# Kernel tuning notes

Measured on AMD Instinct MI355X. Metric: run time of the kernel, lower is better.

The kernel has to match this reference:

```python
import jax, jax.numpy as jnp
import numpy as np
import math

B, S, D, H, FF = 2, 2048, 1024, 16, 4096
DH = D // H


def _layernorm(x, g, b, eps=1e-5):
    mu = jnp.mean(x, axis=-1, keepdims=True)
    var = jnp.mean((x - mu) ** 2, axis=-1, keepdims=True)
    return (x - mu) * jax.lax.rsqrt(var + eps) * g + b


def setup_inputs() -> dict:
    key = jax.random.key(0)
    ks = jax.random.split(key, 16)
    sc = 0.02
    inp = {
        "x": jax.random.normal(ks[0], (B, S, D), dtype=jnp.float32),
        "Wq": jax.random.normal(ks[1], (D, D), dtype=jnp.float32) * sc,
        "bq": jnp.zeros((D,), jnp.float32),
        "Wk": jax.random.normal(ks[2], (D, D), dtype=jnp.float32) * sc,
        "bk": jnp.zeros((D,), jnp.float32),
        "Wv": jax.random.normal(ks[3], (D, D), dtype=jnp.float32) * sc,
        "bv": jnp.zeros((D,), jnp.float32),
        "Wo": jax.random.normal(ks[4], (D, D), dtype=jnp.float32) * sc,
        "bo": jnp.zeros((D,), jnp.float32),
        "Er": jax.random.uniform(ks[5], (S, DH), dtype=jnp.float32),  # torch.rand init
        "W1": jax.random.normal(ks[6], (D, FF), dtype=jnp.float32) * sc,
        "b1": jnp.zeros((FF,), jnp.float32),
        "W2": jax.random.normal(ks[7], (FF, D), dtype=jnp.float32) * sc,
        "b2": jnp.zeros((D,), jnp.float32),
        "g1": jnp.ones((D,), jnp.float32),
        "be1": jnp.zeros((D,), jnp.float32),
        "g2": jnp.ones((D,), jnp.float32),
        "be2": jnp.zeros((D,), jnp.float32),
    }
    return inp


def _skew(qer, m):
    # qer: (B,H,S,S); m: (S,S) flipped upper-triangular mask
    qer = qer * m
    qer = jnp.pad(qer, ((0, 0), (0, 0), (0, 0), (1, 0)))  # (B,H,S,S+1)
    qer = qer.reshape(B, H, S + 1, S)
    return qer[:, :, 1:, :]  # (B,H,S,S)


def reference(x, Wq, bq, Wk, bk, Wv, bv, Wo, bo, Er, W1, b1, W2, b2, g1, be1, g2, be2):
    x1 = _layernorm(x, g1, be1)
    q = ((x1 @ Wq + bq) / math.sqrt(DH)).reshape(B, S, H, DH)
    k = (x1 @ Wk + bk).reshape(B, S, H, DH)
    v = (x1 @ Wv + bv).reshape(B, S, H, DH)
    att = jnp.einsum("bshd,bthd->bhst", q, k)  # (B,H,S,S)
    qer = jnp.einsum("bshd,td->bhst", q, Er)   # (B,H,S,S) since S == max_seq_len
    m = jnp.flip(jnp.triu(jnp.ones((S, S), dtype=x.dtype)), axis=0)
    att = att + _skew(qer, m)
    att = jax.nn.softmax(att, axis=-1)
    out = jnp.einsum("bhst,bthd->bshd", att, v).reshape(B, S, D)
    out = out @ Wo + bo
    x2 = x1 + out
    x3 = _layernorm(x2, g2, be2)
    y = x3 + jax.nn.relu(x3 @ W1 + b1) @ W2 + b2
    return y
```

## Files before the change

kernel.cpp:

```cpp
#include <hip/hip_runtime.h>
#include <stdint.h>

typedef unsigned short u16;
typedef __attribute__((ext_vector_type(8))) short short8;
typedef __attribute__((ext_vector_type(8))) __bf16 bf16x8;
typedef __attribute__((ext_vector_type(4))) float floatx4;

#define AS1 __attribute__((address_space(1)))
#define AS3 __attribute__((address_space(3)))

#define QSCALE 0.18033688f

__device__ __forceinline__ u16 f2bf(float f) {
    union { float f; unsigned u; } v; v.f = f;
    return (u16)((v.u + 0x8000u) >> 16);
}

__device__ __forceinline__ void gl_lds16(const void* g, void* lds) {
    __builtin_amdgcn_global_load_lds((const AS1 unsigned int*)(uintptr_t)g,
                                     (AS3 unsigned int*)(uintptr_t)lds, 16, 0, 0);
}

__device__ __forceinline__ floatx4 mfma16(short8 a, short8 b, floatx4 c) {
    return __builtin_amdgcn_mfma_f32_16x16x32_bf16((bf16x8)a, (bf16x8)b, c, 0, 0, 0);
}

__global__ void transpose4_1024(const float* __restrict__ s0, const float* __restrict__ s1,
                                const float* __restrict__ s2, const float* __restrict__ s3,
                                u16* __restrict__ d) {
    __shared__ float tile[32][33];
    const float* srcs[4] = {s0, s1, s2, s3};
    const float* src = srcs[blockIdx.z];
    u16* dst = d + (size_t)blockIdx.z * 1024 * 1024;
    int c0 = blockIdx.x * 32, r0 = blockIdx.y * 32;
    int tx = threadIdx.x, ty = threadIdx.y;
#pragma unroll
    for (int i = 0; i < 4; i++)
        tile[ty + i * 8][tx] = src[(size_t)(r0 + ty + i * 8) * 1024 + c0 + tx];
    __syncthreads();
#pragma unroll
    for (int i = 0; i < 4; i++)
        dst[(size_t)(c0 + ty + i * 8) * 1024 + r0 + tx] = f2bf(tile[tx][ty + i * 8]);
}

__global__ void transpose_f32_to_bf16(const float* __restrict__ src, u16* __restrict__ dst,
                                      int R, int C) {
    __shared__ float tile[32][33];
    int c0 = blockIdx.x * 32, r0 = blockIdx.y * 32;
    int tx = threadIdx.x, ty = threadIdx.y;
#pragma unroll
    for (int i = 0; i < 4; i++)
        tile[ty + i * 8][tx] = src[(size_t)(r0 + ty + i * 8) * C + c0 + tx];
    __syncthreads();
#pragma unroll
    for (int i = 0; i < 4; i++)
        dst[(size_t)(c0 + ty + i * 8) * R + r0 + tx] = f2bf(tile[tx][ty + i * 8]);
}

__global__ void convert_to_bf16(const float* __restrict__ s, u16* __restrict__ d, int n) {
    int i = blockIdx.x * 256 + threadIdx.x;
    if (i < n) d[i] = f2bf(s[i]);
}

__global__ __launch_bounds__(256) void ln_kernel(const float* __restrict__ x,
                                                 const float* __restrict__ g,
                                                 const float* __restrict__ bt,
                                                 float* __restrict__ yf,
                                                 u16* __restrict__ yb) {
    const int row = blockIdx.x, tid = threadIdx.x;
    const float4 xv = ((const float4*)(x + (size_t)row * 1024))[tid];
    float s = xv.x + xv.y + xv.z + xv.w;
    float sq = xv.x * xv.x + xv.y * xv.y + xv.z * xv.z + xv.w * xv.w;
#pragma unroll
    for (int m = 1; m < 64; m <<= 1) { s += __shfl_xor(s, m); sq += __shfl_xor(sq, m); }
    __shared__ float red[8];
    int w = tid >> 6;
    if ((tid & 63) == 0) { red[w] = s; red[4 + w] = sq; }
    __syncthreads();
    s = red[0] + red[1] + red[2] + red[3];
    sq = red[4] + red[5] + red[6] + red[7];
    float mean = s * (1.f / 1024.f);
    float var = sq * (1.f / 1024.f) - mean * mean;
    float rstd = rsqrtf(var + 1e-5f);
    float4 gv = ((const float4*)g)[tid];
    float4 bv = ((const float4*)bt)[tid];
    float4 y;
    y.x = (xv.x - mean) * rstd * gv.x + bv.x;
    y.y = (xv.y - mean) * rstd * gv.y + bv.y;
    y.z = (xv.z - mean) * rstd * gv.z + bv.z;
    y.w = (xv.w - mean) * rstd * gv.w + bv.w;
    ((float4*)(yf + (size_t)row * 1024))[tid] = y;
    ushort4 u;
    u.x = f2bf(y.x); u.y = f2bf(y.y); u.z = f2bf(y.z); u.w = f2bf(y.w);
    ((ushort4*)(yb + (size_t)row * 1024))[tid] = u;
}

template <int EPI>
__global__ __launch_bounds__(256) void gemm_bt(const u16* __restrict__ A,
                                               const u16* __restrict__ Bt,
                                               const float* __restrict__ bias,
                                               u16* __restrict__ outb,
                                               int M, int N, int K) {
    __shared__ __align__(16) u16 As[128 * 32];
    __shared__ __align__(16) u16 Bs[128 * 32];
    const int tid = threadIdx.x;
    const int w = tid >> 6, l = tid & 63, ln = l & 15, quad = l >> 4;
    const int m0 = blockIdx.y * 128, n0 = blockIdx.x * 128;
    const int wm = (w >> 1) * 64, wn = (w & 1) * 64;
    floatx4 acc[4][4] = {};

    for (int k0 = 0; k0 < K; k0 += 32) {
        __syncthreads();
#pragma unroll
        for (int r = 0; r < 2; r++) {
            int c = tid + r * 256;
            int row = c >> 2, ko = (c & 3) * 8;
            gl_lds16(&A[(size_t)(m0 + row) * K + k0 + ko], &As[(w * 64 + r * 256) * 8]);
            gl_lds16(&Bt[(size_t)(n0 + row) * K + k0 + ko], &Bs[(w * 64 + r * 256) * 8]);
        }
        __syncthreads();
        short8 av[4], bv[4];
#pragma unroll
        for (int mt = 0; mt < 4; mt++)
            av[mt] = *(const short8*)&As[(wm + mt * 16 + ln) * 32 + quad * 8];
#pragma unroll
        for (int nt = 0; nt < 4; nt++)
            bv[nt] = *(const short8*)&Bs[(wn + nt * 16 + ln) * 32 + quad * 8];
#pragma unroll
        for (int mt = 0; mt < 4; mt++)
#pragma unroll
            for (int nt = 0; nt < 4; nt++)
                acc[mt][nt] = mfma16(av[mt], bv[nt], acc[mt][nt]);
    }

#pragma unroll
    for (int nt = 0; nt < 4; nt++) {
        int n = n0 + wn + nt * 16 + ln;
        float bval = bias[n];
#pragma unroll
        for (int mt = 0; mt < 4; mt++) {
#pragma unroll
            for (int r = 0; r < 4; r++) {
                int m = m0 + wm + mt * 16 + quad * 4 + r;
                float v = acc[mt][nt][r] + bval;
                outb[(size_t)m * N + n] = f2bf(fmaxf(v, 0.f));
            }
        }
    }
}

__global__ __launch_bounds__(256) void gemm_qkv(const u16* __restrict__ A,
                                                const u16* __restrict__ Bt,
                                                const float* __restrict__ bq,
                                                const float* __restrict__ bk,
                                                const float* __restrict__ bv,
                                                u16* __restrict__ qb,
                                                u16* __restrict__ kb,
                                                u16* __restrict__ vtb) {
    constexpr int K = 1024;
    __shared__ __align__(16) u16 As[128 * 32];
    __shared__ __align__(16) u16 Bs[128 * 32];
    const int tid = threadIdx.x;
    const int w = tid >> 6, l = tid & 63, ln = l & 15, quad = l >> 4;
    const int m0 = blockIdx.y * 128, n0 = blockIdx.x * 128;
    const int wm = (w >> 1) * 64, wn = (w & 1) * 64;
    floatx4 acc[4][4] = {};

    for (int k0 = 0; k0 < K; k0 += 32) {
        __syncthreads();
#pragma unroll
        for (int r = 0; r < 2; r++) {
            int c = tid + r * 256;
            int row = c >> 2, ko = (c & 3) * 8;
            gl_lds16(&A[(size_t)(m0 + row) * K + k0 + ko], &As[(w * 64 + r * 256) * 8]);
            gl_lds16(&Bt[(size_t)(n0 + row) * K + k0 + ko], &Bs[(w * 64 + r * 256) * 8]);
        }
        __syncthreads();
        short8 av[4], bv4[4];
#pragma unroll
        for (int mt = 0; mt < 4; mt++)
            av[mt] = *(const short8*)&As[(wm + mt * 16 + ln) * 32 + quad * 8];
#pragma unroll
        for (int nt = 0; nt < 4; nt++)
            bv4[nt] = *(const short8*)&Bs[(wn + nt * 16 + ln) * 32 + quad * 8];
#pragma unroll
        for (int mt = 0; mt < 4; mt++)
#pragma unroll
            for (int nt = 0; nt < 4; nt++)
                acc[mt][nt] = mfma16(av[mt], bv4[nt], acc[mt][nt]);
    }

    const int seg = (n0 + wn) >> 10;
#pragma unroll
    for (int nt = 0; nt < 4; nt++) {
        int nl = (n0 + wn + nt * 16 + ln) & 1023;
        float bval = seg == 0 ? bq[nl] : (seg == 1 ? bk[nl] : bv[nl]);
#pragma unroll
        for (int mt = 0; mt < 4; mt++) {
#pragma unroll
            for (int r = 0; r < 4; r++) {
                int m = m0 + wm + mt * 16 + quad * 4 + r;
                float v = acc[mt][nt][r] + bval;
                if (seg == 0) {
                    qb[(size_t)m * 1024 + nl] = f2bf(v * QSCALE);
                } else if (seg == 1) {
                    kb[(size_t)m * 1024 + nl] = f2bf(v);
                } else {
                    int b_ = m >> 11, s = m & 2047, hh = nl >> 6, d = nl & 63;
                    vtb[(((size_t)(b_ * 16 + hh)) * 64 + d) * 2048 + s] = f2bf(v);
                }
            }
        }
    }
}

__global__ __launch_bounds__(256) void gemm_bt64(const u16* __restrict__ A,
                                                 const u16* __restrict__ Bt,
                                                 const float* __restrict__ bias,
                                                 const float* __restrict__ resid,
                                                 float* __restrict__ outf,
                                                 int N, int K) {
    __shared__ __align__(16) u16 As[128 * 32];
    __shared__ __align__(16) u16 Bs[64 * 32];
    const int tid = threadIdx.x;
    const int w = tid >> 6, l = tid & 63, ln = l & 15, quad = l >> 4;
    const int m0 = blockIdx.y * 128, n0 = blockIdx.x * 64;
    const int wm = (w >> 1) * 64, wn = (w & 1) * 32;
    floatx4 acc[4][2] = {};

    for (int k0 = 0; k0 < K; k0 += 32) {
        __syncthreads();
#pragma unroll
        for (int r = 0; r < 2; r++) {
            int c = tid + r * 256;
            int row = c >> 2, ko = (c & 3) * 8;
            gl_lds16(&A[(size_t)(m0 + row) * K + k0 + ko], &As[(w * 64 + r * 256) * 8]);
        }
        {
            int row = tid >> 2, ko = (tid & 3) * 8;
            gl_lds16(&Bt[(size_t)(n0 + row) * K + k0 + ko], &Bs[w * 512]);
        }
        __syncthreads();
        short8 av[4], bv2[2];
#pragma unroll
        for (int mt = 0; mt < 4; mt++)
            av[mt] = *(const short8*)&As[(wm + mt * 16 + ln) * 32 + quad * 8];
#pragma unroll
        for (int nt = 0; nt < 2; nt++)
            bv2[nt] = *(const short8*)&Bs[(wn + nt * 16 + ln) * 32 + quad * 8];
#pragma unroll
        for (int mt = 0; mt < 4; mt++)
#pragma unroll
            for (int nt = 0; nt < 2; nt++)
                acc[mt][nt] = mfma16(av[mt], bv2[nt], acc[mt][nt]);
    }

#pragma unroll
    for (int nt = 0; nt < 2; nt++) {
        int n = n0 + wn + nt * 16 + ln;
        float bval = bias[n];
#pragma unroll
        for (int mt = 0; mt < 4; mt++) {
#pragma unroll
            for (int r = 0; r < 4; r++) {
                int m = m0 + wm + mt * 16 + quad * 4 + r;
                outf[(size_t)m * N + n] = acc[mt][nt][r] + bval + resid[(size_t)m * N + n];
            }
        }
    }
}

__global__ __launch_bounds__(512, 4) void attn_kernel(const u16* __restrict__ qb,
                                                      const u16* __restrict__ kb,
                                                      const u16* __restrict__ vtb,
                                                      const u16* __restrict__ erb,
                                                      u16* __restrict__ ob) {
    constexpr int S = 2048, D = 1024;
    const int s0 = blockIdx.x * 128, h = blockIdx.y, b = blockIdx.z;
    const int tid = threadIdx.x, w = tid >> 6, l = tid & 63, ln = l & 15, quad = l >> 4;

    __shared__ __align__(16) u16 Ks[64 * 64];
    __shared__ __align__(16) u16 Vts[64 * 64];
    __shared__ __align__(16) u16 Ebs[192 * 64];
    __shared__ __align__(16) u16 Ps[8][16 * 72];

    const u16* kbase = kb + ((size_t)b * S) * D + h * 64;
    const u16* vtbase = vtb + ((size_t)(b * 16 + h)) * 64 * S;

    const u16* qrow = qb + ((size_t)b * S + s0 + w * 16 + ln) * D + h * 64;
    short8 aq[2];
    aq[0] = *(const short8*)&qrow[quad * 8];
    aq[1] = *(const short8*)&qrow[32 + quad * 8];

    const short8 ones8 = {16256, 16256, 16256, 16256, 16256, 16256, 16256, 16256};

    int srcl[4], carry[4];
#pragma unroll
    for (int r = 0; r < 4; r++) {
        srcl[r] = (l & 48) | ((ln + 15 - quad * 4 - r) & 15);
        carry[r] = (ln - quad * 4 - r) > 0 ? 1 : 0;
    }

    floatx4 accO[4] = {};
    floatx4 accL = {};
    const int srow_base = s0 + w * 16 + quad * 4;

    for (int t0 = 0; t0 < S; t0 += 64) {
        const bool bias_tile = (t0 <= s0 + 64);
        __syncthreads();
        {
            int row = tid >> 3, sc = (tid & 7) ^ (row & 7);
            gl_lds16(&kbase[(size_t)(t0 + row) * D + sc * 8], &Ks[w * 512]);
            gl_lds16(&vtbase[(size_t)row * S + t0 + sc * 8], &Vts[w * 512]);
        }
        if (bias_tile) {
            int jbase = t0 - s0 + (S - 128);
#pragma unroll
            for (int rr = 0; rr < 3; rr++) {
                int o = tid + rr * 512;
                int row = o >> 3, sc = (o & 7) ^ (row & 7);
                int j = jbase + row; j = j > S - 1 ? S - 1 : j;
                gl_lds16(&erb[(size_t)j * 64 + sc * 8], &Ebs[rr * 4096 + w * 512]);
            }
        }
        __syncthreads();

        floatx4 sacc[4] = {};
#pragma unroll
        for (int kk = 0; kk < 2; kk++)
#pragma unroll
            for (int nt = 0; nt < 4; nt++) {
                int tr = nt * 16 + ln;
                short8 bk = *(const short8*)&Ks[tr * 64 + (((kk * 4 + quad) ^ (tr & 7)) * 8)];
                sacc[nt] = mfma16(aq[kk], bk, sacc[nt]);
            }
        floatx4 gacc[5] = {};
        if (bias_tile) {
#pragma unroll
            for (int kk = 0; kk < 2; kk++)
#pragma unroll
                for (int i = 0; i < 5; i++) {
                    int er = (7 - w + i) * 16 + ln;
                    short8 be = *(const short8*)&Ebs[er * 64 + (((kk * 4 + quad) ^ (er & 7)) * 8)];
                    gacc[i] = mfma16(aq[kk], be, gacc[i]);
                }
        }

#pragma unroll
        for (int r = 0; r < 4; r++) {
            const int rloc = quad * 4 + r;
            const int srow = srow_base + r;
            float sh[5];
            if (bias_tile) {
#pragma unroll
                for (int i = 0; i < 5; i++) sh[i] = __shfl(gacc[i][r], srcl[r]);
            }
#pragma unroll
            for (int nt = 0; nt < 4; nt++) {
                float xv = sacc[nt][r];
                if (bias_tile) {
                    float g = carry[r] ? sh[nt + 1] : sh[nt];
                    bool mk = (t0 + nt * 16 + ln) <= srow;
                    xv += mk ? g : 0.f;
                }
                float p = __builtin_amdgcn_exp2f(xv);
                Ps[w][rloc * 72 + nt * 16 + ln] = f2bf(p);
            }
        }

#pragma unroll
        for (int kk = 0; kk < 2; kk++) {
            short8 pf = *(const short8*)&Ps[w][ln * 72 + kk * 32 + quad * 8];
#pragma unroll
            for (int nt = 0; nt < 4; nt++) {
                int dr = nt * 16 + ln;
                short8 bv = *(const short8*)&Vts[dr * 64 + (((kk * 4 + quad) ^ (dr & 7)) * 8)];
                accO[nt] = mfma16(pf, bv, accO[nt]);
            }
            accL = mfma16(pf, ones8, accL);
        }
    }

#pragma unroll
    for (int r = 0; r < 4; r++) {
        float inv = 1.f / accL[r];
        int srow = srow_base + r;
#pragma unroll
        for (int nt = 0; nt < 4; nt++) {
            ob[((size_t)b * S + srow) * D + h * 64 + nt * 16 + ln] = f2bf(accO[nt][r] * inv);
        }
    }
}

extern "C" void kernel_launch(void* const* d_in, const int* in_sizes, int n_in,
                              void* d_out, int out_size, void* d_ws, size_t ws_size,
                              hipStream_t stream) {
    const float* x   = (const float*)d_in[0];
    const float* Wq  = (const float*)d_in[1];
    const float* bq  = (const float*)d_in[2];
    const float* Wk  = (const float*)d_in[3];
    const float* bk  = (const float*)d_in[4];
    const float* Wv  = (const float*)d_in[5];
    const float* bv  = (const float*)d_in[6];
    const float* Wo  = (const float*)d_in[7];
    const float* bo  = (const float*)d_in[8];
    const float* Er  = (const float*)d_in[9];
    const float* W1  = (const float*)d_in[10];
    const float* b1  = (const float*)d_in[11];
    const float* W2  = (const float*)d_in[12];
    const float* b2  = (const float*)d_in[13];
    const float* g1  = (const float*)d_in[14];
    const float* be1 = (const float*)d_in[15];
    const float* g2  = (const float*)d_in[16];
    const float* be2 = (const float*)d_in[17];
    float* out = (float*)d_out;

    char* ws = (char*)d_ws;
    size_t off = 0;
    auto alloc_f = [&](size_t n) { float* p = (float*)(ws + off); off += n * 4; return p; };
    auto alloc_h = [&](size_t n) { u16* p = (u16*)(ws + off); off += n * 2; return p; };

    float* x1f = alloc_f((size_t)4096 * 1024);
    float* x2f = alloc_f((size_t)4096 * 1024);
    float* x3f = alloc_f((size_t)4096 * 1024);
    u16* x1b = alloc_h((size_t)4096 * 1024);
    u16* x3b = alloc_h((size_t)4096 * 1024);
    u16* qbf = alloc_h((size_t)4096 * 1024);
    u16* kbf = alloc_h((size_t)4096 * 1024);
    u16* vtb = alloc_h((size_t)4096 * 1024);
    u16* aob = alloc_h((size_t)4096 * 1024);
    u16* WqT = alloc_h((size_t)1024 * 1024);
    u16* WkT = alloc_h((size_t)1024 * 1024);
    u16* WvT = alloc_h((size_t)1024 * 1024);
    u16* WoT = alloc_h((size_t)1024 * 1024);
    u16* W1T = alloc_h((size_t)1024 * 4096);
    u16* W2T = alloc_h((size_t)1024 * 4096);
    u16* Erb = alloc_h((size_t)2048 * 64);
    u16* hbf = qbf;
    (void)WkT; (void)WvT;

    dim3 tb(32, 8);
    transpose4_1024<<<dim3(32, 32, 4), tb, 0, stream>>>(Wq, Wk, Wv, Wo, WqT);
    transpose_f32_to_bf16<<<dim3(128, 32), tb, 0, stream>>>(W1, W1T, 1024, 4096);
    transpose_f32_to_bf16<<<dim3(32, 128), tb, 0, stream>>>(W2, W2T, 4096, 1024);
    convert_to_bf16<<<512, 256, 0, stream>>>(Er, Erb, 2048 * 64);

    ln_kernel<<<4096, 256, 0, stream>>>(x, g1, be1, x1f, x1b);

    gemm_qkv<<<dim3(24, 32), 256, 0, stream>>>(x1b, WqT, bq, bk, bv, qbf, kbf, vtb);

    attn_kernel<<<dim3(16, 16, 2), 512, 0, stream>>>(qbf, kbf, vtb, Erb, aob);

    gemm_bt64<<<dim3(16, 32), 256, 0, stream>>>(aob, WoT, bo, x1f, x2f, 1024, 1024);

    ln_kernel<<<4096, 256, 0, stream>>>(x2f, g2, be2, x3f, x3b);

    gemm_bt<3><<<dim3(32, 32), 256, 0, stream>>>(x3b, W1T, b1, hbf, 4096, 4096, 1024);
    gemm_bt64<<<dim3(16, 32), 256, 0, stream>>>(hbf, W2T, b2, x3f, out, 1024, 4096);
}
```

Before: 451.1 us.

## Use K=64 swizzled LDS tiles in GEMMs and split attention key range across waves

All three GEMM kernels now stage K-tiles of 64 instead of 32, with an XOR swizzle on the LDS layout. This halves the number of barrier pairs per K loop and is meant to avoid LDS bank conflicts. The attention kernel now handles 64 query rows per block and splits each 128-key step between two wave groups, merging the partial outputs and row sums through shared memory at the end. It also drops the Er LDS staging in favour of direct global loads and raises the occupancy hint. These changes add LDS use and a final reduction, and the direct Er loads may be less coalesced.

```diff
diff --git a/kernel.cpp b/kernel.cpp
--- a/kernel.cpp
+++ b/kernel.cpp
@@ -95,42 +95,48 @@
     ((ushort4*)(yb + (size_t)row * 1024))[tid] = u;
 }
 
-template <int EPI>
 __global__ __launch_bounds__(256) void gemm_bt(const u16* __restrict__ A,
                                                const u16* __restrict__ Bt,
                                                const float* __restrict__ bias,
                                                u16* __restrict__ outb,
                                                int M, int N, int K) {
-    __shared__ __align__(16) u16 As[128 * 32];
-    __shared__ __align__(16) u16 Bs[128 * 32];
+    __shared__ __align__(16) u16 As[128 * 64];
+    __shared__ __align__(16) u16 Bs[128 * 64];
     const int tid = threadIdx.x;
     const int w = tid >> 6, l = tid & 63, ln = l & 15, quad = l >> 4;
     const int m0 = blockIdx.y * 128, n0 = blockIdx.x * 128;
     const int wm = (w >> 1) * 64, wn = (w & 1) * 64;
     floatx4 acc[4][4] = {};
 
-    for (int k0 = 0; k0 < K; k0 += 32) {
-        __syncthreads();
-#pragma unroll
-        for (int r = 0; r < 2; r++) {
-            int c = tid + r * 256;
-            int row = c >> 2, ko = (c & 3) * 8;
-            gl_lds16(&A[(size_t)(m0 + row) * K + k0 + ko], &As[(w * 64 + r * 256) * 8]);
-            gl_lds16(&Bt[(size_t)(n0 + row) * K + k0 + ko], &Bs[(w * 64 + r * 256) * 8]);
-        }
-        __syncthreads();
-        short8 av[4], bv[4];
-#pragma unroll
-        for (int mt = 0; mt < 4; mt++)
-            av[mt] = *(const short8*)&As[(wm + mt * 16 + ln) * 32 + quad * 8];
-#pragma unroll
-        for (int nt = 0; nt < 4; nt++)
-            bv[nt] = *(const short8*)&Bs[(wn + nt * 16 + ln) * 32 + quad * 8];
-#pragma unroll
-        for (int mt = 0; mt < 4; mt++)
-#pragma unroll
-            for (int nt = 0; nt < 4; nt++)
-                acc[mt][nt] = mfma16(av[mt], bv[nt], acc[mt][nt]);
+    for (int k0 = 0; k0 < K; k0 += 64) {
+        __syncthreads();
+#pragma unroll
+        for (int r = 0; r < 4; r++) {
+            int o = tid + r * 256;
+            int row = o >> 3, c = (o & 7) ^ (row & 7);
+            gl_lds16(&A[(size_t)(m0 + row) * K + k0 + c * 8], &As[(w * 64 + r * 256) * 8]);
+            gl_lds16(&Bt[(size_t)(n0 + row) * K + k0 + c * 8], &Bs[(w * 64 + r * 256) * 8]);
+        }
+        __syncthreads();
+#pragma unroll
+        for (int kk = 0; kk < 2; kk++) {
+            short8 av[4], bv[4];
+#pragma unroll
+            for (int mt = 0; mt < 4; mt++) {
+                int rr = wm + mt * 16 + ln;
+                av[mt] = *(const short8*)&As[rr * 64 + (((kk * 4 + quad) ^ (rr & 7)) * 8)];
+            }
+#pragma unroll
+            for (int nt = 0; nt < 4; nt++) {
+                int rr = wn + nt * 16 + ln;
+                bv[nt] = *(const short8*)&Bs[rr * 64 + (((kk * 4 + quad) ^ (rr & 7)) * 8)];
+            }
+#pragma unroll
+            for (int mt = 0; mt < 4; mt++)
+#pragma unroll
+                for (int nt = 0; nt < 4; nt++)
+                    acc[mt][nt] = mfma16(av[mt], bv[nt], acc[mt][nt]);
+        }
     }
 
 #pragma unroll
@@ -158,36 +164,43 @@
                                                 u16* __restrict__ kb,
                                                 u16* __restrict__ vtb) {
     constexpr int K = 1024;
-    __shared__ __align__(16) u16 As[128 * 32];
-    __shared__ __align__(16) u16 Bs[128 * 32];
+    __shared__ __align__(16) u16 As[128 * 64];
+    __shared__ __align__(16) u16 Bs[128 * 64];
     const int tid = threadIdx.x;
     const int w = tid >> 6, l = tid & 63, ln = l & 15, quad = l >> 4;
     const int m0 = blockIdx.y * 128, n0 = blockIdx.x * 128;
     const int wm = (w >> 1) * 64, wn = (w & 1) * 64;
     floatx4 acc[4][4] = {};
 
-    for (int k0 = 0; k0 < K; k0 += 32) {
-        __syncthreads();
-#pragma unroll
-        for (int r = 0; r < 2; r++) {
-            int c = tid + r * 256;
-            int row = c >> 2, ko = (c & 3) * 8;
-            gl_lds16(&A[(size_t)(m0 + row) * K + k0 + ko], &As[(w * 64 + r * 256) * 8]);
-            gl_lds16(&Bt[(size_t)(n0 + row) * K + k0 + ko], &Bs[(w * 64 + r * 256) * 8]);
-        }
-        __syncthreads();
-        short8 av[4], bv4[4];
-#pragma unroll
-        for (int mt = 0; mt < 4; mt++)
-            av[mt] = *(const short8*)&As[(wm + mt * 16 + ln) * 32 + quad * 8];
-#pragma unroll
-        for (int nt = 0; nt < 4; nt++)
-            bv4[nt] = *(const short8*)&Bs[(wn + nt * 16 + ln) * 32 + quad * 8];
-#pragma unroll
-        for (int mt = 0; mt < 4; mt++)
-#pragma unroll
-            for (int nt = 0; nt < 4; nt++)
-                acc[mt][nt] = mfma16(av[mt], bv4[nt], acc[mt][nt]);
+    for (int k0 = 0; k0 < K; k0 += 64) {
+        __syncthreads();
+#pragma unroll
+        for (int r = 0; r < 4; r++) {
+            int o = tid + r * 256;
+            int row = o >> 3, c = (o & 7) ^ (row & 7);
+            gl_lds16(&A[(size_t)(m0 + row) * K + k0 + c * 8], &As[(w * 64 + r * 256) * 8]);
+            gl_lds16(&Bt[(size_t)(n0 + row) * K + k0 + c * 8], &Bs[(w * 64 + r * 256) * 8]);
+        }
+        __syncthreads();
+#pragma unroll
+        for (int kk = 0; kk < 2; kk++) {
+            short8 av[4], bv4[4];
+#pragma unroll
+            for (int mt = 0; mt < 4; mt++) {
+                int rr = wm + mt * 16 + ln;
+                av[mt] = *(const short8*)&As[rr * 64 + (((kk * 4 + quad) ^ (rr & 7)) * 8)];
+            }
+#pragma unroll
+            for (int nt = 0; nt < 4; nt++) {
+                int rr = wn + nt * 16 + ln;
+                bv4[nt] = *(const short8*)&Bs[rr * 64 + (((kk * 4 + quad) ^ (rr & 7)) * 8)];
+            }
+#pragma unroll
+            for (int mt = 0; mt < 4; mt++)
+#pragma unroll
+                for (int nt = 0; nt < 4; nt++)
+                    acc[mt][nt] = mfma16(av[mt], bv4[nt], acc[mt][nt]);
+        }
     }
 
     const int seg = (n0 + wn) >> 10;
@@ -220,39 +233,48 @@
                                                  const float* __restrict__ resid,
                                                  float* __restrict__ outf,
                                                  int N, int K) {
-    __shared__ __align__(16) u16 As[128 * 32];
-    __shared__ __align__(16) u16 Bs[64 * 32];
+    __shared__ __align__(16) u16 As[128 * 64];
+    __shared__ __align__(16) u16 Bs[64 * 64];
     const int tid = threadIdx.x;
     const int w = tid >> 6, l = tid & 63, ln = l & 15, quad = l >> 4;
     const int m0 = blockIdx.y * 128, n0 = blockIdx.x * 64;
     const int wm = (w >> 1) * 64, wn = (w & 1) * 32;
     floatx4 acc[4][2] = {};
 
-    for (int k0 = 0; k0 < K; k0 += 32) {
-        __syncthreads();
+    for (int k0 = 0; k0 < K; k0 += 64) {
+        __syncthreads();
+#pragma unroll
+        for (int r = 0; r < 4; r++) {
+            int o = tid + r * 256;
+            int row = o >> 3, c = (o & 7) ^ (row & 7);
+            gl_lds16(&A[(size_t)(m0 + row) * K + k0 + c * 8], &As[(w * 64 + r * 256) * 8]);
+        }
 #pragma unroll
         for (int r = 0; r < 2; r++) {
-            int c = tid + r * 256;
-            int row = c >> 2, ko = (c & 3) * 8;
-            gl_lds16(&A[(size_t)(m0 + row) * K + k0 + ko], &As[(w * 64 + r * 256) * 8]);
-        }
-        {
-            int row = tid >> 2, ko = (tid & 3) * 8;
-            gl_lds16(&Bt[(size_t)(n0 + row) * K + k0 + ko], &Bs[w * 512]);
-        }
-        __syncthreads();
-        short8 av[4], bv2[2];
-#pragma unroll
-        for (int mt = 0; mt < 4; mt++)
-            av[mt] = *(const short8*)&As[(wm + mt * 16 + ln) * 32 + quad * 8];
-#pragma unroll
-        for (int nt = 0; nt < 2; nt++)
-            bv2[nt] = *(const short8*)&Bs[(wn + nt * 16 + ln) * 32 + quad * 8];
-#pragma unroll
-        for (int mt = 0; mt < 4; mt++)
-#pragma unroll
-            for (int nt = 0; nt < 2; nt++)
-                acc[mt][nt] = mfma16(av[mt], bv2[nt], acc[mt][nt]);
+            int o = tid + r * 256;
+            int row = o >> 3, c = (o & 7) ^ (row & 7);
+            gl_lds16(&Bt[(size_t)(n0 + row) * K + k0 + c * 8], &Bs[(w * 64 + r * 256) * 8]);
+        }
+        __syncthreads();
+#pragma unroll
+        for (int kk = 0; kk < 2; kk++) {
+            short8 av[4], bv2[2];
+#pragma unroll
+            for (int mt = 0; mt < 4; mt++) {
+                int rr = wm + mt * 16 + ln;
+                av[mt] = *(const short8*)&As[rr * 64 + (((kk * 4 + quad) ^ (rr & 7)) * 8)];
+            }
+#pragma unroll
+            for (int nt = 0; nt < 2; nt++) {
+                int rr = wn + nt * 16 + ln;
+                bv2[nt] = *(const short8*)&Bs[rr * 64 + (((kk * 4 + quad) ^ (rr & 7)) * 8)];
+            }
+#pragma unroll
+            for (int mt = 0; mt < 4; mt++)
+#pragma unroll
+                for (int nt = 0; nt < 2; nt++)
+                    acc[mt][nt] = mfma16(av[mt], bv2[nt], acc[mt][nt]);
+        }
     }
 
 #pragma unroll
@@ -270,24 +292,24 @@
     }
 }
 
-__global__ __launch_bounds__(512, 4) void attn_kernel(const u16* __restrict__ qb,
+__global__ __launch_bounds__(512, 6) void attn_kernel(const u16* __restrict__ qb,
                                                       const u16* __restrict__ kb,
                                                       const u16* __restrict__ vtb,
                                                       const u16* __restrict__ erb,
                                                       u16* __restrict__ ob) {
     constexpr int S = 2048, D = 1024;
-    const int s0 = blockIdx.x * 128, h = blockIdx.y, b = blockIdx.z;
+    const int s0 = blockIdx.x * 64, h = blockIdx.y, b = blockIdx.z;
     const int tid = threadIdx.x, w = tid >> 6, l = tid & 63, ln = l & 15, quad = l >> 4;
-
-    __shared__ __align__(16) u16 Ks[64 * 64];
-    __shared__ __align__(16) u16 Vts[64 * 64];
-    __shared__ __align__(16) u16 Ebs[192 * 64];
+    const int qw = w & 3, tw = w >> 2;
+
+    __shared__ __align__(16) u16 Ks[2][64 * 64];
+    __shared__ __align__(16) u16 Vts[2][64 * 64];
     __shared__ __align__(16) u16 Ps[8][16 * 72];
 
     const u16* kbase = kb + ((size_t)b * S) * D + h * 64;
     const u16* vtbase = vtb + ((size_t)(b * 16 + h)) * 64 * S;
 
-    const u16* qrow = qb + ((size_t)b * S + s0 + w * 16 + ln) * D + h * 64;
+    const u16* qrow = qb + ((size_t)b * S + s0 + qw * 16 + ln) * D + h * 64;
     short8 aq[2];
     aq[0] = *(const short8*)&qrow[quad * 8];
     aq[1] = *(const short8*)&qrow[32 + quad * 8];
@@ -303,24 +325,19 @@
 
     floatx4 accO[4] = {};
     floatx4 accL = {};
-    const int srow_base = s0 + w * 16 + quad * 4;
-
-    for (int t0 = 0; t0 < S; t0 += 64) {
-        const bool bias_tile = (t0 <= s0 + 64);
+    const int srow_base = s0 + qw * 16 + quad * 4;
+
+    for (int it = 0; it < S / 128; it++) {
+        const int t0 = it * 128 + tw * 64;
+        const bool bias_tile = (t0 <= s0);
         __syncthreads();
         {
             int row = tid >> 3, sc = (tid & 7) ^ (row & 7);
-            gl_lds16(&kbase[(size_t)(t0 + row) * D + sc * 8], &Ks[w * 512]);
-            gl_lds16(&vtbase[(size_t)row * S + t0 + sc * 8], &Vts[w * 512]);
-        }
-        if (bias_tile) {
-            int jbase = t0 - s0 + (S - 128);
-#pragma unroll
-            for (int rr = 0; rr < 3; rr++) {
-                int o = tid + rr * 512;
-                int row = o >> 3, sc = (o & 7) ^ (row & 7);
-                int j = jbase + row; j = j > S - 1 ? S - 1 : j;
-                gl_lds16(&erb[(size_t)j * 64 + sc * 8], &Ebs[rr * 4096 + w * 512]);
+#pragma unroll
+            for (int tt = 0; tt < 2; tt++) {
+                int tg = it * 128 + tt * 64;
+                gl_lds16(&kbase[(size_t)(tg + row) * D + sc * 8], &Ks[tt][w * 512]);
+                gl_lds16(&vtbase[(size_t)row * S + tg + sc * 8], &Vts[tt][w * 512]);
             }
         }
         __syncthreads();
@@ -331,19 +348,22 @@
 #pragma unroll
             for (int nt = 0; nt < 4; nt++) {
                 int tr = nt * 16 + ln;
-                short8 bk = *(const short8*)&Ks[tr * 64 + (((kk * 4 + quad) ^ (tr & 7)) * 8)];
+                short8 bk = *(const short8*)&Ks[tw][tr * 64 + (((kk * 4 + quad) ^ (tr & 7)) * 8)];
                 sacc[nt] = mfma16(aq[kk], bk, sacc[nt]);
             }
         floatx4 gacc[5] = {};
         if (bias_tile) {
-#pragma unroll
-            for (int kk = 0; kk < 2; kk++)
-#pragma unroll
-                for (int i = 0; i < 5; i++) {
-                    int er = (7 - w + i) * 16 + ln;
-                    short8 be = *(const short8*)&Ebs[er * 64 + (((kk * 4 + quad) ^ (er & 7)) * 8)];
-                    gacc[i] = mfma16(aq[kk], be, gacc[i]);
-                }
+            int jw0 = t0 - s0 - qw * 16 + 2032;
+#pragma unroll
+            for (int i = 0; i < 5; i++) {
+                int j = jw0 + i * 16 + ln;
+                j = j > S - 1 ? S - 1 : j;
+                const u16* ep = erb + (size_t)j * 64;
+                short8 e0 = *(const short8*)&ep[quad * 8];
+                short8 e1 = *(const short8*)&ep[32 + quad * 8];
+                gacc[i] = mfma16(aq[0], e0, gacc[i]);
+                gacc[i] = mfma16(aq[1], e1, gacc[i]);
+            }
         }
 
 #pragma unroll
@@ -374,20 +394,39 @@
 #pragma unroll
             for (int nt = 0; nt < 4; nt++) {
                 int dr = nt * 16 + ln;
-                short8 bv = *(const short8*)&Vts[dr * 64 + (((kk * 4 + quad) ^ (dr & 7)) * 8)];
+                short8 bv = *(const short8*)&Vts[tw][dr * 64 + (((kk * 4 + quad) ^ (dr & 7)) * 8)];
                 accO[nt] = mfma16(pf, bv, accO[nt]);
             }
             accL = mfma16(pf, ones8, accL);
         }
     }
 
-#pragma unroll
-    for (int r = 0; r < 4; r++) {
-        float inv = 1.f / accL[r];
-        int srow = srow_base + r;
-#pragma unroll
-        for (int nt = 0; nt < 4; nt++) {
-            ob[((size_t)b * S + srow) * D + h * 64 + nt * 16 + ln] = f2bf(accO[nt][r] * inv);
+    __syncthreads();
+    float* Om = (float*)&Ks[0][0];
+    float* Lm = (float*)&Vts[0][0];
+    if (tw == 1) {
+#pragma unroll
+        for (int nt = 0; nt < 4; nt++)
+#pragma unroll
+            for (int r = 0; r < 4; r++)
+                Om[(qw * 16 + quad * 4 + r) * 64 + nt * 16 + ln] = accO[nt][r];
+        if (ln == 0) {
+#pragma unroll
+            for (int r = 0; r < 4; r++) Lm[qw * 16 + quad * 4 + r] = accL[r];
+        }
+    }
+    __syncthreads();
+    if (tw == 0) {
+#pragma unroll
+        for (int r = 0; r < 4; r++) {
+            float lsum = accL[r] + Lm[qw * 16 + quad * 4 + r];
+            float inv = 1.f / lsum;
+            int srow = srow_base + r;
+#pragma unroll
+            for (int nt = 0; nt < 4; nt++) {
+                float val = (accO[nt][r] + Om[(qw * 16 + quad * 4 + r) * 64 + nt * 16 + ln]) * inv;
+                ob[((size_t)b * S + srow) * D + h * 64 + nt * 16 + ln] = f2bf(val);
+            }
         }
     }
 }
@@ -449,12 +488,12 @@
 
     gemm_qkv<<<dim3(24, 32), 256, 0, stream>>>(x1b, WqT, bq, bk, bv, qbf, kbf, vtb);
 
-    attn_kernel<<<dim3(16, 16, 2), 512, 0, stream>>>(qbf, kbf, vtb, Erb, aob);
+    attn_kernel<<<dim3(32, 16, 2), 512, 0, stream>>>(qbf, kbf, vtb, Erb, aob);
 
     gemm_bt64<<<dim3(16, 32), 256, 0, stream>>>(aob, WoT, bo, x1f, x2f, 1024, 1024);
 
     ln_kernel<<<4096, 256, 0, stream>>>(x2f, g2, be2, x3f, x3b);
 
-    gemm_bt<3><<<dim3(32, 32), 256, 0, stream>>>(x3b, W1T, b1, hbf, 4096, 4096, 1024);
+    gemm_bt<<<dim3(32, 32), 256, 0, stream>>>(x3b, W1T, b1, hbf, 4096, 4096, 1024);
     gemm_bt64<<<dim3(16, 32), 256, 0, stream>>>(hbf, W2T, b2, x3f, out, 1024, 4096);
 }
```

Result: slower. 647.6 us (+43.6%).
